# Optimization experiments

Measured on AMD Instinct MI355X. Metric: run time of the kernel, lower is better.

## Reference

```python
import jax, jax.numpy as jnp
import numpy as np


def _unfold3(x):
    # x: (B, 1, H, W) -> (B, 9, L), L=(H-2)*(W-2); kernel positions row-major (matches torch Unfold)
    B, _, H, W = x.shape
    patches = jnp.stack(
        [x[:, 0, i:H - 2 + i, j:W - 2 + j] for i in range(3) for j in range(3)], axis=1
    )  # (B, 9, H-2, W-2)
    return patches.reshape(B, 9, (H - 2) * (W - 2))


def setup_inputs() -> dict:
    key = jax.random.key(0)
    k1, k2, k3 = jax.random.split(key, 3)
    B, H, Wd = 16, 64, 64
    D = 32  # dendrite
    x = jax.random.uniform(k1, (B, 1, H, Wd), dtype=jnp.float32) * 255.0
    W = 0.01 * jnp.abs(jax.random.normal(k2, (D, 18, 4), dtype=jnp.float32)) + 0.2
    q = 0.01 * jnp.abs(jax.random.normal(k3, (D, 18, 4), dtype=jnp.float32)) + 0.0
    return {"x": x, "W": W, "q": q}


def reference(x, W, q):
    K_SYN = 10.0   # DConvSynaps k
    K_SOMA = 10.0  # DConvSoma slope
    p = _unfold3(x)                   # (B, 9, L)
    center = p[:, 4:5, :]             # (B, 1, L) center pixel of each 3x3 patch
    # torch.isclose(p, center, rtol=0, atol=3) -> |p - center| <= 3
    x1 = (jnp.abs(p - center) <= 3.0).astype(p.dtype)
    x1 = x1.at[:, 4, :].set(1.0)
    feat = jnp.concatenate([x1, p], axis=1)            # (B, 18, L)
    # DConvSynaps broadcast: (B, L, 1, 18, 1) against W,q (D, 18, 4)
    xb = feat.transpose(0, 2, 1)[:, :, None, :, None]  # (B, L, 1, 18, 1)
    syn = jax.nn.sigmoid((xb * W - q) * K_SYN)         # (B, L, D, 18, 4)
    dend = jnp.prod(syn, axis=3)                       # (B, L, D, 4)
    menb = jnp.sum(dend, axis=2)                       # (B, L, 4)
    soma = jax.nn.sigmoid((menb - 0.5) * K_SOMA)       # (B, L, 4)
    return jnp.sum(soma, axis=1)                       # (B, 4)
```

## Files before the change

kernel.cpp:

```cpp
#include <hip/hip_runtime.h>
#include <math.h>

#define LOG2E 1.44269504088896340736f

constexpr int IMG  = 64;
constexpr int OW   = 62;
constexpr int NPIX = 62 * 62;
constexpr int D    = 32;
constexpr int K    = 4;
constexpr int CHUNKS = (NPIX + 63) / 64;

__global__ __launch_bounds__(256, 4)
void orientation_kernel(const float* __restrict__ x,
                        const float* __restrict__ Wm,
                        const float* __restrict__ qm,
                        float* __restrict__ out)
{
    __shared__ float4 tbl[K * D * 9];

    const int tid = threadIdx.x;

    for (int t = tid; t < K * D * 9; t += 256) {
        const int j = t % 9;
        const int dk = t / 9;
        const int d = dk % D;
        const int k = dk / D;
        const int base = d * 72;

        const float w0 = Wm[base + j * 4 + k];
        const float q0 = qm[base + j * 4 + k];
        const float s1 = __builtin_amdgcn_rcpf(
            1.f + __builtin_amdgcn_exp2f(-10.f * LOG2E * (w0 - q0)));
        float s0, ds;
        if (j == 4) {
            s0 = s1; ds = 0.f;
        } else {
            s0 = __builtin_amdgcn_rcpf(
                1.f + __builtin_amdgcn_exp2f(10.f * LOG2E * q0));
            ds = s1 - s0;
        }
        const float w1 = Wm[base + (9 + j) * 4 + k];
        const float q1 = qm[base + (9 + j) * 4 + k];
        tbl[t] = make_float4(s0, ds, -10.f * LOG2E * w1, 10.f * LOG2E * q1);
    }
    __syncthreads();

    const int lane = tid & 63;
    const int k    = tid >> 6;
    const int b     = blockIdx.x / CHUNKS;
    const int chunk = blockIdx.x - b * CHUNKS;

    const int pi    = chunk * 64 + lane;
    const bool valid = (pi < NPIX);
    const int pic   = valid ? pi : (NPIX - 1);
    const int row   = pic / OW;
    const int col   = pic - row * OW;

    const float* xb = x + b * IMG * IMG;
    float p[9];
#pragma unroll
    for (int i = 0; i < 3; ++i)
#pragma unroll
        for (int jj = 0; jj < 3; ++jj)
            p[i * 3 + jj] = xb[(row + i) * IMG + col + jj];

    const float ctr = p[4];
    float x1f[9];
#pragma unroll
    for (int j = 0; j < 9; ++j)
        x1f[j] = (fabsf(p[j] - ctr) <= 3.0f) ? 1.f : 0.f;

    const float4* tk = &tbl[k * D * 9];
    float menb = 0.f;
#pragma unroll 2
    for (int d = 0; d < D; ++d) {
        float prodB = 1.f;
        float prodA = 1.f;
#pragma unroll
        for (int j = 0; j < 9; ++j) {
            const float4 c = tk[d * 9 + j];
            prodB *= fmaf(x1f[j], c.y, c.x);
            const float e = __builtin_amdgcn_exp2f(fmaf(p[j], c.z, c.w));
            prodA = fmaf(prodA, e, prodA);
        }
        menb += prodB * __builtin_amdgcn_rcpf(prodA);
    }

    float soma = __builtin_amdgcn_rcpf(
        1.f + __builtin_amdgcn_exp2f((0.5f - menb) * (10.f * LOG2E)));
    if (!valid) soma = 0.f;

#pragma unroll
    for (int m = 1; m <= 32; m <<= 1)
        soma += __shfl_xor(soma, m, 64);

    if (lane == 0)
        atomicAdd(&out[b * 4 + k], soma);
}

extern "C" void kernel_launch(void* const* d_in, const int* in_sizes, int n_in,
                              void* d_out, int out_size, void* d_ws, size_t ws_size,
                              hipStream_t stream) {
    const float* x  = (const float*)d_in[0];
    const float* Wm = (const float*)d_in[1];
    const float* qm = (const float*)d_in[2];
    float* out = (float*)d_out;

    const int B = in_sizes[0] / (IMG * IMG);

    hipMemsetAsync(d_out, 0, (size_t)out_size * sizeof(float), stream);

    dim3 grid(B * CHUNKS);
    dim3 block(256);
    orientation_kernel<<<grid, block, 0, stream>>>(x, Wm, qm, out);
}
```

Measured before the change: 45.35 us.

## Precompute log-domain synapse table in separate kernel, read it from global memory

Moves construction of the per-(k,d) synapse constants into a separate single-block kernel that writes them to workspace. The binary-feature product is rewritten as a sum of logs followed by one exp2, and the analog term is refactored to use a precomputed exp of the bias. The main kernel now runs 64-thread blocks, one per (pixel chunk, k), reading constants straight from global memory instead of shared memory. This drops the per-block table build and sync, at the cost of an extra kernel launch and global/scalar-cache loads for the table.

```diff
diff --git a/kernel.cpp b/kernel.cpp
--- a/kernel.cpp
+++ b/kernel.cpp
@@ -3,52 +3,57 @@
 
 #define LOG2E 1.44269504088896340736f
 
-constexpr int IMG  = 64;
-constexpr int OW   = 62;
-constexpr int NPIX = 62 * 62;
-constexpr int D    = 32;
-constexpr int K    = 4;
+constexpr int IMG    = 64;
+constexpr int OW     = 62;
+constexpr int NPIX   = OW * OW;
+constexpr int D      = 32;
+constexpr int K      = 4;
 constexpr int CHUNKS = (NPIX + 63) / 64;
+constexpr int TSTR   = 32;
 
-__global__ __launch_bounds__(256, 4)
-void orientation_kernel(const float* __restrict__ x,
-                        const float* __restrict__ Wm,
-                        const float* __restrict__ qm,
-                        float* __restrict__ out)
+__global__ void build_table(const float* __restrict__ Wm,
+                            const float* __restrict__ qm,
+                            float* __restrict__ tb)
 {
-    __shared__ float4 tbl[K * D * 9];
+    const int t = threadIdx.x;
+    if (t >= K * D) return;
+    const int d = t & 31;
+    const int k = t >> 5;
+    const int base = d * 72;
+    float* e = tb + t * TSTR;
 
-    const int tid = threadIdx.x;
-
-    for (int t = tid; t < K * D * 9; t += 256) {
-        const int j = t % 9;
-        const int dk = t / 9;
-        const int d = dk % D;
-        const int k = dk / D;
-        const int base = d * 72;
-
+    float cB = 0.f;
+    int jj = 0;
+    for (int j = 0; j < 9; ++j) {
         const float w0 = Wm[base + j * 4 + k];
         const float q0 = qm[base + j * 4 + k];
-        const float s1 = __builtin_amdgcn_rcpf(
-            1.f + __builtin_amdgcn_exp2f(-10.f * LOG2E * (w0 - q0)));
-        float s0, ds;
+        const float s1 = 1.f / (1.f + expf(-10.f * (w0 - q0)));
         if (j == 4) {
-            s0 = s1; ds = 0.f;
+            cB += log2f(s1);
         } else {
-            s0 = __builtin_amdgcn_rcpf(
-                1.f + __builtin_amdgcn_exp2f(10.f * LOG2E * q0));
-            ds = s1 - s0;
+            const float s0 = 1.f / (1.f + expf(10.f * q0));
+            cB += log2f(s0);
+            e[jj++] = log2f(s1) - log2f(s0);
         }
         const float w1 = Wm[base + (9 + j) * 4 + k];
         const float q1 = qm[base + (9 + j) * 4 + k];
-        tbl[t] = make_float4(s0, ds, -10.f * LOG2E * w1, 10.f * LOG2E * q1);
+        e[8 + 2 * j]     = -10.f * LOG2E * w1;
+        e[8 + 2 * j + 1] = expf(10.f * q1);
     }
-    __syncthreads();
+    e[26] = cB;
+}
 
-    const int lane = tid & 63;
-    const int k    = tid >> 6;
-    const int b     = blockIdx.x / CHUNKS;
-    const int chunk = blockIdx.x - b * CHUNKS;
+__global__ __launch_bounds__(64)
+void orientation_main(const float* __restrict__ x,
+                      const float* __restrict__ tb,
+                      float* __restrict__ out)
+{
+    const int lane = threadIdx.x;
+    int blk = blockIdx.x;
+    const int k = blk & 3;
+    blk >>= 2;
+    const int b     = blk / CHUNKS;
+    const int chunk = blk - b * CHUNKS;
 
     const int pi    = chunk * 64 + lane;
     const bool valid = (pi < NPIX);
@@ -61,29 +66,42 @@
 #pragma unroll
     for (int i = 0; i < 3; ++i)
 #pragma unroll
-        for (int jj = 0; jj < 3; ++jj)
-            p[i * 3 + jj] = xb[(row + i) * IMG + col + jj];
+        for (int jc = 0; jc < 3; ++jc)
+            p[i * 3 + jc] = xb[(row + i) * IMG + col + jc];
 
     const float ctr = p[4];
-    float x1f[9];
+    float x1v[9];
 #pragma unroll
     for (int j = 0; j < 9; ++j)
-        x1f[j] = (fabsf(p[j] - ctr) <= 3.0f) ? 1.f : 0.f;
+        x1v[j] = (fabsf(p[j] - ctr) <= 3.0f) ? 1.f : 0.f;
 
-    const float4* tk = &tbl[k * D * 9];
+    const float* tk = tb + (k * D) * TSTR;
+
     float menb = 0.f;
-#pragma unroll 2
+#pragma unroll 4
     for (int d = 0; d < D; ++d) {
-        float prodB = 1.f;
+        const float* e = tk + d * TSTR;
+
+        float logB = e[26];
+        logB = fmaf(x1v[0], e[0], logB);
+        logB = fmaf(x1v[1], e[1], logB);
+        logB = fmaf(x1v[2], e[2], logB);
+        logB = fmaf(x1v[3], e[3], logB);
+        logB = fmaf(x1v[5], e[4], logB);
+        logB = fmaf(x1v[6], e[5], logB);
+        logB = fmaf(x1v[7], e[6], logB);
+        logB = fmaf(x1v[8], e[7], logB);
+
         float prodA = 1.f;
 #pragma unroll
         for (int j = 0; j < 9; ++j) {
-            const float4 c = tk[d * 9 + j];
-            prodB *= fmaf(x1f[j], c.y, c.x);
-            const float e = __builtin_amdgcn_exp2f(fmaf(p[j], c.z, c.w));
-            prodA = fmaf(prodA, e, prodA);
+            const float E = __builtin_amdgcn_exp2f(p[j] * e[8 + 2 * j]);
+            const float t = prodA * E;
+            prodA = fmaf(t, e[9 + 2 * j], prodA);
         }
-        menb += prodB * __builtin_amdgcn_rcpf(prodA);
+
+        menb = fmaf(__builtin_amdgcn_exp2f(logB),
+                    __builtin_amdgcn_rcpf(prodA), menb);
     }
 
     float soma = __builtin_amdgcn_rcpf(
@@ -105,12 +123,15 @@
     const float* Wm = (const float*)d_in[1];
     const float* qm = (const float*)d_in[2];
     float* out = (float*)d_out;
+    float* tb  = (float*)d_ws;
 
     const int B = in_sizes[0] / (IMG * IMG);
 
     hipMemsetAsync(d_out, 0, (size_t)out_size * sizeof(float), stream);
 
-    dim3 grid(B * CHUNKS);
-    dim3 block(256);
-    orientation_kernel<<<grid, block, 0, stream>>>(x, Wm, qm, out);
+    build_table<<<1, 128, 0, stream>>>(Wm, qm, tb);
+
+    dim3 grid(B * CHUNKS * K);
+    dim3 block(64);
+    orientation_main<<<grid, block, 0, stream>>>(x, tb, out);
 }
```

New measurement: 49.46 us. +9.0%, slower.
